# Kernel optimization log

Measured on AMD Instinct MI355X. Metric: run time of the kernel, lower is better.

The kernel has to match this reference:

```python
import jax, jax.numpy as jnp
import numpy as np

N = 50000
NEG_SLOPE = 0.2  # PyG GATConv default
EPS = 1e-16      # PyG softmax denominator epsilon


def gat_conv(x, src, dst, W, a_src, a_dst, b):
    """Single-head PyG-style GATConv. src/dst already include self-loops."""
    h = x @ W                                   # [N, out]
    alpha_s = h @ a_src                         # [N]
    alpha_d = h @ a_dst                         # [N]
    e = alpha_s[src] + alpha_d[dst]             # [E]
    e = jnp.where(e >= 0, e, NEG_SLOPE * e)     # LeakyReLU
    # segment softmax over incoming edges of each dst node
    m = jax.ops.segment_max(e, dst, num_segments=N)
    ex = jnp.exp(e - m[dst])
    denom = jax.ops.segment_sum(ex, dst, num_segments=N)
    alpha = ex / (denom[dst] + EPS)             # [E]
    out = jax.ops.segment_sum(h[src] * alpha[:, None], dst, num_segments=N)
    return out + b


def add_self_loops(edge_index):
    loop = jnp.arange(N, dtype=edge_index.dtype)
    src = jnp.concatenate([edge_index[0], loop])
    dst = jnp.concatenate([edge_index[1], loop])
    return src, dst


def setup_inputs() -> dict:
    key = jax.random.key(0)
    ks = jax.random.split(key, 10)
    F_in, H, C, E = 128, 128, 16, 800000
    x = jax.random.normal(ks[0], (N, F_in), dtype=jnp.float32)
    edge_index = jax.random.randint(ks[1], (2, E), 0, N, dtype=jnp.int64)
    s1 = 1.0 / np.sqrt(F_in)
    s2 = 1.0 / np.sqrt(H)
    W1 = jax.random.uniform(ks[2], (F_in, H), jnp.float32, -s1, s1)
    a_src1 = jax.random.uniform(ks[3], (H,), jnp.float32, -s2, s2)
    a_dst1 = jax.random.uniform(ks[4], (H,), jnp.float32, -s2, s2)
    b1 = jnp.zeros((H,), jnp.float32)
    W2 = jax.random.uniform(ks[5], (H, C), jnp.float32, -s2, s2)
    sc = 1.0 / np.sqrt(C)
    a_src2 = jax.random.uniform(ks[6], (C,), jnp.float32, -sc, sc)
    a_dst2 = jax.random.uniform(ks[7], (C,), jnp.float32, -sc, sc)
    b2 = jnp.zeros((C,), jnp.float32)
    return {"x": x, "edge_index": edge_index, "W1": W1, "a_src1": a_src1,
            "a_dst1": a_dst1, "b1": b1, "W2": W2, "a_src2": a_src2,
            "a_dst2": a_dst2, "b2": b2}


def reference(x, edge_index, W1, a_src1, a_dst1, b1, W2, a_src2, a_dst2, b2):
    src, dst = add_self_loops(edge_index)
    h = gat_conv(x, src, dst, W1, a_src1, a_dst1, b1)
    h = jax.nn.relu(h)
    # dropout is identity at inference (droprate applied only in training)
    out = gat_conv(h, src, dst, W2, a_src2, a_dst2, b2)
    return jax.nn.log_softmax(out, axis=1)
```

## Files before the change

kernel.cpp:

```cpp
#include <hip/hip_runtime.h>
#include <math.h>

#define NODES 50000
#define NEDGE 800000
#define ETOT  (NEDGE + NODES)
#define CAP   96
#define GROWS 64
#define GBLK  ((NODES + GROWS - 1) / GROWS)
#define BSH   10
#define NBUCK ((NODES + 1023) / 1024)
#define BCAP  24576
#define SCAP  20480

typedef unsigned short ushort_t;
typedef unsigned int uint_t;
typedef __attribute__((ext_vector_type(8))) short bf16x8;
typedef __attribute__((ext_vector_type(4))) float f32x4;

__device__ __forceinline__ ushort_t f2bf(float f) {
    uint_t u = __float_as_uint(f);
    return (ushort_t)((u + 0x7fffu + ((u >> 16) & 1u)) >> 16);
}
__device__ __forceinline__ uint_t pack2bf(float a, float b) {
    return (uint_t)f2bf(a) | ((uint_t)f2bf(b) << 16);
}

__global__ void gemm_xw_alpha(const float* __restrict__ X, const float* __restrict__ W,
                              const float* __restrict__ a_src, const float* __restrict__ a_dst,
                              ushort_t* __restrict__ Hb, float* __restrict__ as_,
                              float* __restrict__ ad_, int n) {
    __shared__ __align__(16) ushort_t wt[128][136];
    __shared__ float asl[128], adl[128];
    const int t = threadIdx.x;
    #pragma unroll
    for (int i = 0; i < 16; ++i) {
        int idx = i * 256 + t;
        int k = idx >> 5, c4 = (idx & 31) * 4;
        float4 w = *(const float4*)(W + (size_t)k * 128 + c4);
        wt[c4 + 0][k] = f2bf(w.x);
        wt[c4 + 1][k] = f2bf(w.y);
        wt[c4 + 2][k] = f2bf(w.z);
        wt[c4 + 3][k] = f2bf(w.w);
    }
    if (t < 128) { asl[t] = a_src[t]; adl[t] = a_dst[t]; }
    __syncthreads();

    const int lane = t & 63, wid = t >> 6;
    const int r0 = blockIdx.x * GROWS + wid * 16;
    const int arow = r0 + (lane & 15);
    const int kq = (lane >> 4) * 8;

    bf16x8 afrag[4];
    #pragma unroll
    for (int ks = 0; ks < 4; ++ks) {
        union { bf16x8 v; uint_t u[4]; } af;
        if (arow < n) {
            const float* xp = X + (size_t)arow * 128 + ks * 32 + kq;
            float4 xa = *(const float4*)(xp);
            float4 xb = *(const float4*)(xp + 4);
            af.u[0] = pack2bf(xa.x, xa.y); af.u[1] = pack2bf(xa.z, xa.w);
            af.u[2] = pack2bf(xb.x, xb.y); af.u[3] = pack2bf(xb.z, xb.w);
        } else {
            af.u[0] = af.u[1] = af.u[2] = af.u[3] = 0u;
        }
        afrag[ks] = af.v;
    }

    f32x4 acc[8];
    #pragma unroll
    for (int c = 0; c < 8; ++c) { acc[c].x = 0.f; acc[c].y = 0.f; acc[c].z = 0.f; acc[c].w = 0.f; }
    #pragma unroll
    for (int c = 0; c < 8; ++c) {
        #pragma unroll
        for (int ks = 0; ks < 4; ++ks) {
            const bf16x8 bfrag = *(const bf16x8*)(&wt[c * 16 + (lane & 15)][ks * 32 + kq]);
            acc[c] = __builtin_amdgcn_mfma_f32_16x16x32_bf16(afrag[ks], bfrag, acc[c], 0, 0, 0);
        }
    }

    const int q = lane >> 4, cl = lane & 15;
    #pragma unroll
    for (int r = 0; r < 4; ++r) {
        int row = r0 + q * 4 + r;
        bool ok = row < n;
        float s = 0.f, d = 0.f;
        #pragma unroll
        for (int c = 0; c < 8; ++c) {
            float v = (r == 0) ? acc[c].x : (r == 1) ? acc[c].y : (r == 2) ? acc[c].z : acc[c].w;
            if (ok) Hb[(size_t)row * 128 + c * 16 + cl] = f2bf(v);
            s += v * asl[c * 16 + cl];
            d += v * adl[c * 16 + cl];
        }
        #pragma unroll
        for (int off = 1; off < 16; off <<= 1) {
            s += __shfl_xor(s, off);
            d += __shfl_xor(d, off);
        }
        if (cl == 0 && ok) { as_[row] = s; ad_[row] = d; }
    }
}

__global__ void bin_pass1(const int* __restrict__ ei, int* __restrict__ bcnt,
                          uint_t* __restrict__ packed) {
    __shared__ int lh[NBUCK];
    __shared__ int gbase_[NBUCK];
    const int t = threadIdx.x;
    const int e0 = blockIdx.x * 1024;
    if (t < NBUCK) lh[t] = 0;
    __syncthreads();
    int s[4], d[4], bk[4];
    const int eb = e0 + 4 * t;
    if (eb + 3 < NEDGE) {
        int4 sv = *(const int4*)(ei + eb);
        int4 dv = *(const int4*)(ei + NEDGE + eb);
        s[0] = sv.x; s[1] = sv.y; s[2] = sv.z; s[3] = sv.w;
        d[0] = dv.x; d[1] = dv.y; d[2] = dv.z; d[3] = dv.w;
        #pragma unroll
        for (int j = 0; j < 4; ++j) bk[j] = d[j] >> BSH;
    } else {
        #pragma unroll
        for (int j = 0; j < 4; ++j) {
            int e = eb + j;
            if (e >= ETOT) { bk[j] = -1; }
            else if (e < NEDGE) { s[j] = ei[e]; d[j] = ei[NEDGE + e]; bk[j] = d[j] >> BSH; }
            else { s[j] = d[j] = e - NEDGE; bk[j] = d[j] >> BSH; }
        }
    }
    #pragma unroll
    for (int j = 0; j < 4; ++j)
        if (bk[j] >= 0) atomicAdd(&lh[bk[j]], 1);
    __syncthreads();
    if (t < NBUCK) {
        int c = lh[t];
        gbase_[t] = c ? atomicAdd(&bcnt[t], c) : 0;
        lh[t] = 0;
    }
    __syncthreads();
    #pragma unroll
    for (int j = 0; j < 4; ++j) {
        if (bk[j] >= 0) {
            int lpos = atomicAdd(&lh[bk[j]], 1);
            int pos = gbase_[bk[j]] + lpos;
            if (pos < BCAP)
                packed[(size_t)bk[j] * BCAP + pos] = ((uint_t)d[j] << 16) | (uint_t)s[j];
        }
    }
}

__global__ void bin_pass2(const int* __restrict__ bcnt, const uint_t* __restrict__ packed,
                          int* __restrict__ rowptr, ushort_t* __restrict__ srcs) {
    __shared__ ushort_t sbuf[SCAP];
    __shared__ int lcnt[1024], lexc[1024];
    __shared__ int wsum[4];
    __shared__ int gbs_s;
    const int t = threadIdx.x;
    const int b = blockIdx.x;
    const int n0 = b << BSH;
    const int nEnd = (n0 + 1024 < NODES) ? n0 + 1024 : NODES;
    const int cnt = bcnt[b];
    const uint_t* pk = packed + (size_t)b * BCAP;
    if (t < 64) {
        int c = (t < NBUCK) ? bcnt[t] : 0;
        int sv = c;
        #pragma unroll
        for (int off = 1; off < 64; off <<= 1) {
            int o = __shfl_up(sv, off);
            if (t >= off) sv += o;
        }
        if (t == b) gbs_s = sv - c;
    }
    for (int i = t; i < 1024; i += 256) lcnt[i] = 0;
    __syncthreads();
    for (int i = t; i < cnt; i += 256) {
        int dl = (int)(pk[i] >> 16) - n0;
        atomicAdd(&lcnt[dl], 1);
    }
    __syncthreads();
    int c0 = lcnt[4 * t], c1 = lcnt[4 * t + 1], c2 = lcnt[4 * t + 2], c3 = lcnt[4 * t + 3];
    int s4 = c0 + c1 + c2 + c3;
    int lane = t & 63, wv = t >> 6;
    int sv = s4;
    #pragma unroll
    for (int off = 1; off < 64; off <<= 1) {
        int o = __shfl_up(sv, off);
        if (lane >= off) sv += o;
    }
    if (lane == 63) wsum[wv] = sv;
    __syncthreads();
    int add = 0;
    for (int j = 0; j < wv; ++j) add += wsum[j];
    int base = add + sv - s4;
    lexc[4 * t]     = base;
    lexc[4 * t + 1] = base + c0;
    lexc[4 * t + 2] = base + c0 + c1;
    lexc[4 * t + 3] = base + c0 + c1 + c2;
    const int gb = gbs_s;
    #pragma unroll
    for (int j = 0; j < 4; ++j) {
        int nn = n0 + 4 * t + j;
        if (nn < nEnd) rowptr[nn] = gb + lexc[4 * t + j];
    }
    if (b == NBUCK - 1 && t == 255) rowptr[NODES] = gb + cnt;
    __syncthreads();
    for (int i = t; i < 1024; i += 256) lcnt[i] = lexc[i];
    __syncthreads();
    if (cnt <= SCAP) {
        for (int i = t; i < cnt; i += 256) {
            uint_t e = pk[i];
            int dl = (int)(e >> 16) - n0;
            int lp = atomicAdd(&lcnt[dl], 1);
            sbuf[lp] = (ushort_t)(e & 0xffffu);
        }
        __syncthreads();
        for (int i = t; i < cnt; i += 256)
            srcs[(size_t)gb + i] = sbuf[i];
    } else {
        for (int i = t; i < cnt; i += 256) {
            uint_t e = pk[i];
            int dl = (int)(e >> 16) - n0;
            int lp = atomicAdd(&lcnt[dl], 1);
            srcs[(size_t)gb + lp] = (ushort_t)(e & 0xffffu);
        }
    }
}

__global__ void gat_fused128(const int* __restrict__ rowptr, const ushort_t* __restrict__ srcs,
                             const float* __restrict__ as_, const float* __restrict__ ad_,
                             const ushort_t* __restrict__ Hb, const float* __restrict__ b,
                             ushort_t* __restrict__ outb) {
    __shared__ float sw[4][CAP];
    __shared__ int   ss[4][CAP];
    int wid = (blockIdx.x * blockDim.x + threadIdx.x) >> 6;
    int lane = threadIdx.x & 63;
    int wv = (threadIdx.x >> 6) & 3;
    if (wid >= NODES) return;
    const int beg = rowptr[wid], deg = rowptr[wid + 1] - beg;
    const float adv = ad_[wid];
    float den = 0.f;
    for (int i = lane; i < deg; i += 64) {
        int s = srcs[beg + i];
        float v = as_[s] + adv;
        v = (v >= 0.f) ? v : 0.2f * v;
        float w = __expf(v);
        if (i < CAP) { sw[wv][i] = w; ss[wv][i] = s; }
        den += w;
    }
    #pragma unroll
    for (int off = 32; off; off >>= 1) den += __shfl_xor(den, off);
    const float invd = 1.f / (den + 1e-16f);
    float ax = 0.f, ay = 0.f;
    const int nl = deg < CAP ? deg : CAP;
    int i = 0;
    for (; i + 8 <= nl; i += 8) {
        uint_t u[8];
        float w[8];
        #pragma unroll
        for (int j = 0; j < 8; ++j) {
            w[j] = sw[wv][i + j];
            u[j] = *(const uint_t*)(Hb + (size_t)ss[wv][i + j] * 128 + lane * 2);
        }
        #pragma unroll
        for (int j = 0; j < 8; ++j) {
            ax += w[j] * __uint_as_float(u[j] << 16);
            ay += w[j] * __uint_as_float(u[j] & 0xffff0000u);
        }
    }
    for (; i + 4 <= nl; i += 4) {
        uint_t u[4];
        float w[4];
        #pragma unroll
        for (int j = 0; j < 4; ++j) {
            w[j] = sw[wv][i + j];
            u[j] = *(const uint_t*)(Hb + (size_t)ss[wv][i + j] * 128 + lane * 2);
        }
        #pragma unroll
        for (int j = 0; j < 4; ++j) {
            ax += w[j] * __uint_as_float(u[j] << 16);
            ay += w[j] * __uint_as_float(u[j] & 0xffff0000u);
        }
    }
    for (; i < nl; ++i) {
        float w0 = sw[wv][i];
        uint_t u0 = *(const uint_t*)(Hb + (size_t)ss[wv][i] * 128 + lane * 2);
        ax += w0 * __uint_as_float(u0 << 16);
        ay += w0 * __uint_as_float(u0 & 0xffff0000u);
    }
    for (int j = CAP; j < deg; ++j) {
        int s0 = srcs[beg + j];
        float v = as_[s0] + adv; v = (v >= 0.f) ? v : 0.2f * v;
        float w0 = __expf(v);
        uint_t u0 = *(const uint_t*)(Hb + (size_t)s0 * 128 + lane * 2);
        ax += w0 * __uint_as_float(u0 << 16);
        ay += w0 * __uint_as_float(u0 & 0xffff0000u);
    }
    float ox = fmaxf(ax * invd + b[lane * 2], 0.f);
    float oy = fmaxf(ay * invd + b[lane * 2 + 1], 0.f);
    uint_t pk = (uint_t)f2bf(ox) | ((uint_t)f2bf(oy) << 16);
    *(uint_t*)(outb + (size_t)wid * 128 + lane * 2) = pk;
}

__global__ void gemm_hw2_alpha(const ushort_t* __restrict__ Hinb, const float* __restrict__ W,
                               const float* __restrict__ a_src, const float* __restrict__ a_dst,
                               float* __restrict__ Hout, float* __restrict__ as_,
                               float* __restrict__ ad_, int n) {
    __shared__ float wl[128 * 16];
    for (int i = threadIdx.x; i < 128 * 16; i += 256) wl[i] = W[i];
    __syncthreads();
    int tid = blockIdx.x * blockDim.x + threadIdx.x;
    int node = tid >> 4, col = tid & 15;
    if (node >= n) return;
    const uint4* hr = (const uint4*)(Hinb + (size_t)node * 128);
    float acc = 0.f;
    #pragma unroll
    for (int i = 0; i < 16; ++i) {
        uint4 q = hr[i];
        int k = i * 8;
        acc += __uint_as_float(q.x << 16)          * wl[(k + 0) * 16 + col];
        acc += __uint_as_float(q.x & 0xffff0000u)  * wl[(k + 1) * 16 + col];
        acc += __uint_as_float(q.y << 16)          * wl[(k + 2) * 16 + col];
        acc += __uint_as_float(q.y & 0xffff0000u)  * wl[(k + 3) * 16 + col];
        acc += __uint_as_float(q.z << 16)          * wl[(k + 4) * 16 + col];
        acc += __uint_as_float(q.z & 0xffff0000u)  * wl[(k + 5) * 16 + col];
        acc += __uint_as_float(q.w << 16)          * wl[(k + 6) * 16 + col];
        acc += __uint_as_float(q.w & 0xffff0000u)  * wl[(k + 7) * 16 + col];
    }
    Hout[(size_t)node * 16 + col] = acc;
    float ps = acc * a_src[col], pd = acc * a_dst[col];
    #pragma unroll
    for (int off = 1; off < 16; off <<= 1) {
        ps += __shfl_xor(ps, off);
        pd += __shfl_xor(pd, off);
    }
    if (col == 0) { as_[node] = ps; ad_[node] = pd; }
}

__global__ void gat_fused16_lsm(const int* __restrict__ rowptr, const ushort_t* __restrict__ srcs,
                                const float* __restrict__ as_, const float* __restrict__ ad_,
                                const float* __restrict__ H, const float* __restrict__ b,
                                float* __restrict__ out) {
    __shared__ float sw[4][CAP];
    __shared__ int   ss[4][CAP];
    int wid = (blockIdx.x * blockDim.x + threadIdx.x) >> 6;
    int lane = threadIdx.x & 63;
    int wv = (threadIdx.x >> 6) & 3;
    int slot = lane >> 4, k = lane & 15;
    if (wid >= NODES) return;
    const int beg = rowptr[wid], deg = rowptr[wid + 1] - beg;
    const float adv = ad_[wid];
    float den = 0.f;
    for (int i = lane; i < deg; i += 64) {
        int s = srcs[beg + i];
        float v = as_[s] + adv;
        v = (v >= 0.f) ? v : 0.2f * v;
        float w = __expf(v);
        if (i < CAP) { sw[wv][i] = w; ss[wv][i] = s; }
        den += w;
    }
    #pragma unroll
    for (int off = 32; off; off >>= 1) den += __shfl_xor(den, off);
    const float invd = 1.f / (den + 1e-16f);
    float acc = 0.f;
    const int nl = deg < CAP ? deg : CAP;
    int i = slot;
    for (; i + 4 < nl; i += 8) {
        float w0 = sw[wv][i],     w1 = sw[wv][i + 4];
        float h0 = H[(size_t)ss[wv][i] * 16 + k];
        float h1 = H[(size_t)ss[wv][i + 4] * 16 + k];
        acc += w0 * h0 + w1 * h1;
    }
    if (i < nl) acc += sw[wv][i] * H[(size_t)ss[wv][i] * 16 + k];
    for (int j = CAP + slot; j < deg; j += 4) {
        int s = srcs[beg + j];
        float v = as_[s] + adv; v = (v >= 0.f) ? v : 0.2f * v;
        acc += __expf(v) * H[(size_t)s * 16 + k];
    }
    acc += __shfl_xor(acc, 16);
    acc += __shfl_xor(acc, 32);
    float v = acc * invd + b[k];
    float mx = v;
    #pragma unroll
    for (int off = 1; off < 16; off <<= 1) mx = fmaxf(mx, __shfl_xor(mx, off));
    float ex = __expf(v - mx), ssum = ex;
    #pragma unroll
    for (int off = 1; off < 16; off <<= 1) ssum += __shfl_xor(ssum, off);
    float r = v - mx - __logf(ssum);
    if (lane < 16) out[(size_t)wid * 16 + k] = r;
}

extern "C" void kernel_launch(void* const* d_in, const int* in_sizes, int n_in,
                              void* d_out, int out_size, void* d_ws, size_t ws_size,
                              hipStream_t stream) {
    const float* x      = (const float*)d_in[0];
    const int*   ei     = (const int*)d_in[1];
    const float* W1     = (const float*)d_in[2];
    const float* a_src1 = (const float*)d_in[3];
    const float* a_dst1 = (const float*)d_in[4];
    const float* b1     = (const float*)d_in[5];
    const float* W2     = (const float*)d_in[6];
    const float* a_src2 = (const float*)d_in[7];
    const float* a_dst2 = (const float*)d_in[8];
    const float* b2     = (const float*)d_in[9];
    float* out = (float*)d_out;

    float* p = (float*)d_ws;
    ushort_t* h1b   = (ushort_t*)p; p += (size_t)NODES * 64;
    ushort_t* agg1b = (ushort_t*)p; p += (size_t)NODES * 64;
    float* h2     = p; p += (size_t)NODES * 16;
    float* as_    = p; p += NODES;
    float* ad_    = p; p += NODES;
    float* as2    = p; p += NODES;
    float* ad2    = p; p += NODES;
    uint_t* packed = (uint_t*)p; p += (size_t)NBUCK * BCAP;
    int* ip = (int*)p;
    int* rowptr = ip; ip += NODES + 1;
    int* bcnt   = ip; ip += 64;
    ushort_t* srcs = (ushort_t*)ip;

    const int WAVEGRID = (NODES * 64 + 255) / 256;

    hipMemsetAsync(bcnt, 0, 64 * sizeof(int), stream);
    bin_pass1<<<(ETOT + 1023) / 1024, 256, 0, stream>>>(ei, bcnt, packed);
    bin_pass2<<<NBUCK, 256, 0, stream>>>(bcnt, packed, rowptr, srcs);

    gemm_xw_alpha<<<GBLK, 256, 0, stream>>>(x, W1, a_src1, a_dst1, h1b, as_, ad_, NODES);
    gat_fused128<<<WAVEGRID, 256, 0, stream>>>(rowptr, srcs, as_, ad_, h1b, b1, agg1b);

    gemm_hw2_alpha<<<(NODES * 16 + 255) / 256, 256, 0, stream>>>(agg1b, W2, a_src2, a_dst2, h2, as2, ad2, NODES);
    gat_fused16_lsm<<<WAVEGRID, 256, 0, stream>>>(rowptr, srcs, as2, ad2, h2, b2, out);
}
```

Before: 154.3 us.

## Fuse layer-2 GEMM and attention logits into layer-1 aggregation kernel

The layer-1 aggregation kernel now applies bias and ReLU, stages each node's 128-wide output in shared memory, and multiplies it by W2 (transposed into padded LDS) to produce h2 plus the layer-2 source/destination attention scalars directly. This removes the bf16 intermediate agg1 buffer write and re-read, and one kernel launch. In exchange, every block reloads W2 into LDS, LDS use per block rises (which may lower occupancy), and the per-wave 32-step dot product adds compute to an already gather-bound kernel. Precision also changes slightly, since the intermediate is no longer rounded to bf16.

Measured after the change: 153.3 us. No clear change (-0.6%).

```diff
diff --git a/kernel.cpp b/kernel.cpp
--- a/kernel.cpp
+++ b/kernel.cpp
@@ -226,13 +226,27 @@
 
 __global__ void gat_fused128(const int* __restrict__ rowptr, const ushort_t* __restrict__ srcs,
                              const float* __restrict__ as_, const float* __restrict__ ad_,
-                             const ushort_t* __restrict__ Hb, const float* __restrict__ b,
-                             ushort_t* __restrict__ outb) {
+                             const ushort_t* __restrict__ Hb, const float* __restrict__ b1,
+                             const float* __restrict__ W2, const float* __restrict__ a_src2,
+                             const float* __restrict__ a_dst2,
+                             float* __restrict__ h2, float* __restrict__ as2,
+                             float* __restrict__ ad2) {
+    __shared__ float wt2[16][132];
+    __shared__ float al2s[16], al2d[16];
     __shared__ float sw[4][CAP];
     __shared__ int   ss[4][CAP];
-    int wid = (blockIdx.x * blockDim.x + threadIdx.x) >> 6;
-    int lane = threadIdx.x & 63;
-    int wv = (threadIdx.x >> 6) & 3;
+    __shared__ float ov[4][128];
+    const int t = threadIdx.x;
+    for (int i = t; i < 2048; i += 256) {
+        int c = i & 15, k = i >> 4;
+        wt2[c][k] = W2[k * 16 + c];
+    }
+    if (t < 16) { al2s[t] = a_src2[t]; al2d[t] = a_dst2[t]; }
+    __syncthreads();
+
+    int wid = (blockIdx.x * blockDim.x + t) >> 6;
+    int lane = t & 63;
+    int wv = (t >> 6) & 3;
     if (wid >= NODES) return;
     const int beg = rowptr[wid], deg = rowptr[wid + 1] - beg;
     const float adv = ad_[wid];
@@ -293,45 +307,26 @@
         ax += w0 * __uint_as_float(u0 << 16);
         ay += w0 * __uint_as_float(u0 & 0xffff0000u);
     }
-    float ox = fmaxf(ax * invd + b[lane * 2], 0.f);
-    float oy = fmaxf(ay * invd + b[lane * 2 + 1], 0.f);
-    uint_t pk = (uint_t)f2bf(ox) | ((uint_t)f2bf(oy) << 16);
-    *(uint_t*)(outb + (size_t)wid * 128 + lane * 2) = pk;
-}
-
-__global__ void gemm_hw2_alpha(const ushort_t* __restrict__ Hinb, const float* __restrict__ W,
-                               const float* __restrict__ a_src, const float* __restrict__ a_dst,
-                               float* __restrict__ Hout, float* __restrict__ as_,
-                               float* __restrict__ ad_, int n) {
-    __shared__ float wl[128 * 16];
-    for (int i = threadIdx.x; i < 128 * 16; i += 256) wl[i] = W[i];
-    __syncthreads();
-    int tid = blockIdx.x * blockDim.x + threadIdx.x;
-    int node = tid >> 4, col = tid & 15;
-    if (node >= n) return;
-    const uint4* hr = (const uint4*)(Hinb + (size_t)node * 128);
-    float acc = 0.f;
-    #pragma unroll
-    for (int i = 0; i < 16; ++i) {
-        uint4 q = hr[i];
-        int k = i * 8;
-        acc += __uint_as_float(q.x << 16)          * wl[(k + 0) * 16 + col];
-        acc += __uint_as_float(q.x & 0xffff0000u)  * wl[(k + 1) * 16 + col];
-        acc += __uint_as_float(q.y << 16)          * wl[(k + 2) * 16 + col];
-        acc += __uint_as_float(q.y & 0xffff0000u)  * wl[(k + 3) * 16 + col];
-        acc += __uint_as_float(q.z << 16)          * wl[(k + 4) * 16 + col];
-        acc += __uint_as_float(q.z & 0xffff0000u)  * wl[(k + 5) * 16 + col];
-        acc += __uint_as_float(q.w << 16)          * wl[(k + 6) * 16 + col];
-        acc += __uint_as_float(q.w & 0xffff0000u)  * wl[(k + 7) * 16 + col];
-    }
-    Hout[(size_t)node * 16 + col] = acc;
-    float ps = acc * a_src[col], pd = acc * a_dst[col];
+    const float ox = fmaxf(ax * invd + b1[lane * 2], 0.f);
+    const float oy = fmaxf(ay * invd + b1[lane * 2 + 1], 0.f);
+    *(float2*)(&ov[wv][lane * 2]) = make_float2(ox, oy);
+    const int col = lane & 15, part = lane >> 4;
+    float pacc = 0.f;
+    #pragma unroll
+    for (int kk = 0; kk < 32; ++kk) {
+        int k = part * 32 + kk;
+        pacc += ov[wv][k] * wt2[col][k];
+    }
+    pacc += __shfl_xor(pacc, 16);
+    pacc += __shfl_xor(pacc, 32);
+    if (lane < 16) h2[(size_t)wid * 16 + col] = pacc;
+    float ps = pacc * al2s[col], pd = pacc * al2d[col];
     #pragma unroll
     for (int off = 1; off < 16; off <<= 1) {
         ps += __shfl_xor(ps, off);
         pd += __shfl_xor(pd, off);
     }
-    if (col == 0) { as_[node] = ps; ad_[node] = pd; }
+    if (lane == 0) { as2[wid] = ps; ad2[wid] = pd; }
 }
 
 __global__ void gat_fused16_lsm(const int* __restrict__ rowptr, const ushort_t* __restrict__ srcs,
@@ -403,8 +398,7 @@
     float* out = (float*)d_out;
 
     float* p = (float*)d_ws;
-    ushort_t* h1b   = (ushort_t*)p; p += (size_t)NODES * 64;
-    ushort_t* agg1b = (ushort_t*)p; p += (size_t)NODES * 64;
+    ushort_t* h1b = (ushort_t*)p; p += (size_t)NODES * 64;
     float* h2     = p; p += (size_t)NODES * 16;
     float* as_    = p; p += NODES;
     float* ad_    = p; p += NODES;
@@ -423,8 +417,9 @@
     bin_pass2<<<NBUCK, 256, 0, stream>>>(bcnt, packed, rowptr, srcs);
 
     gemm_xw_alpha<<<GBLK, 256, 0, stream>>>(x, W1, a_src1, a_dst1, h1b, as_, ad_, NODES);
-    gat_fused128<<<WAVEGRID, 256, 0, stream>>>(rowptr, srcs, as_, ad_, h1b, b1, agg1b);
-
-    gemm_hw2_alpha<<<(NODES * 16 + 255) / 256, 256, 0, stream>>>(agg1b, W2, a_src2, a_dst2, h2, as2, ad2, NODES);
+
+    gat_fused128<<<WAVEGRID, 256, 0, stream>>>(rowptr, srcs, as_, ad_, h1b, b1,
+                                               W2, a_src2, a_dst2, h2, as2, ad2);
+
     gat_fused16_lsm<<<WAVEGRID, 256, 0, stream>>>(rowptr, srcs, as2, ad2, h2, b2, out);
 }
```
